# Kernel optimization log

Measured on AMD Instinct MI355X. Metric: run time of the kernel, lower is better.

Reference implementation:

```python
import jax, jax.numpy as jnp
import numpy as np

B, L, J, D_IN, D_OUT = 64, 243, 17, 256, 256
EPS = 1e-5


def _skeleton_adjacency(num_joints=17):
    edges = [(0, 1), (1, 2), (2, 3), (0, 4), (4, 5), (5, 6), (0, 7), (7, 8), (8, 9),
             (9, 10), (8, 11), (11, 12), (12, 13), (1, 14), (14, 15), (1, 16), (16, 17)]
    adj = np.zeros((num_joints, num_joints), dtype=np.float32)
    for u, v in edges:
        if u < num_joints and v < num_joints:
            adj[u, v] = 1.0
            adj[v, u] = 1.0
    np.fill_diagonal(adj, 1.0)
    d = adj.sum(axis=1) ** (-0.5)
    return (d[:, None] * adj) * d[None, :]


def setup_inputs() -> dict:
    key = jax.random.key(0)
    ks = jax.random.split(key, 8)
    s_in = 1.0 / np.sqrt(D_IN)
    s_out = 1.0 / np.sqrt(D_OUT)
    s_h = 1.0 / np.sqrt(2 * D_OUT)
    return {
        "x": jax.random.normal(ks[0], (B, L, J, D_IN), dtype=jnp.float32),
        "adj": jnp.asarray(_skeleton_adjacency(J)),
        "w1": jax.random.normal(ks[1], (D_OUT, D_IN), dtype=jnp.float32) * s_in,
        "b1": jnp.zeros((D_OUT,), dtype=jnp.float32),
        "w2": jax.random.normal(ks[2], (D_OUT, D_IN), dtype=jnp.float32) * s_in,
        "b2": jnp.zeros((D_OUT,), dtype=jnp.float32),
        "bn_gamma": jnp.ones((D_OUT,), dtype=jnp.float32),
        "bn_beta": jnp.zeros((D_OUT,), dtype=jnp.float32),
        "ln_gamma": jnp.ones((D_OUT,), dtype=jnp.float32),
        "ln_beta": jnp.zeros((D_OUT,), dtype=jnp.float32),
        "mlp_w1": jax.random.normal(ks[3], (2 * D_OUT, D_OUT), dtype=jnp.float32) * s_out,
        "mlp_b1": jnp.zeros((2 * D_OUT,), dtype=jnp.float32),
        "mlp_w2": jax.random.normal(ks[4], (D_OUT, 2 * D_OUT), dtype=jnp.float32) * s_h,
        "mlp_b2": jnp.zeros((D_OUT,), dtype=jnp.float32),
    }


def reference(x, adj, w1, b1, w2, b2, bn_gamma, bn_beta, ln_gamma, ln_beta,
              mlp_w1, mlp_b1, mlp_w2, mlp_b2):
    b, l, j, d = x.shape
    xf = x.reshape(b * l, j, d)  # [BL, J, D]
    # two linear projections, each aggregated over joints by the (symmetric)
    # normalized adjacency: out1 uses adj^T, out2 uses adj
    o1 = jnp.einsum("njd,od->njo", xf, w1) + b1
    o1 = jnp.einsum("ji,njo->nio", adj, o1)  # adj.T aggregation
    o2 = jnp.einsum("njd,od->njo", xf, w2) + b2
    o2 = jnp.einsum("ij,njo->nio", adj, o2)
    h = jax.nn.relu(o1 + o2)  # [BL, J, Dout]
    # BatchNorm1d over flattened (BL*J) rows, biased variance (training mode)
    mu = h.mean(axis=(0, 1))
    var = jnp.mean(jnp.square(h - mu), axis=(0, 1))
    h = (h - mu) * jax.lax.rsqrt(var + EPS) * bn_gamma + bn_beta
    # LayerNorm over channel dim
    lmu = h.mean(axis=-1, keepdims=True)
    lvar = jnp.mean(jnp.square(h - lmu), axis=-1, keepdims=True)
    hn = (h - lmu) * jax.lax.rsqrt(lvar + EPS) * ln_gamma + ln_beta
    # MLP: Linear -> ReLU -> Linear
    mid = jax.nn.relu(jnp.einsum("njo,ho->njh", hn, mlp_w1) + mlp_b1)
    out = jnp.einsum("njh,oh->njo", mid, mlp_w2) + mlp_b2
    return out.reshape(b, l, j, -1)
```

## Files before the change

### kernel.cpp

```cpp
#include <hip/hip_runtime.h>
#include <hip/hip_bf16.h>

#define NGRP 15552
#define RROWS 264384
#define EPSV 1e-5f

typedef __attribute__((ext_vector_type(8))) short s16x8;
typedef __attribute__((ext_vector_type(4))) float f32x4;
typedef __hip_bfloat16 bf16;

__device__ __forceinline__ float bf2f(unsigned short u) {
    union { unsigned int i; float f; } x; x.i = ((unsigned int)u) << 16; return x.f;
}
__device__ __forceinline__ unsigned short f2bf(float f) {
    bf16 b = __float2bfloat16(f);
    return *reinterpret_cast<unsigned short*>(&b);
}

__global__ __launch_bounds__(256)
void k_prep(const float* __restrict__ w1, const float* __restrict__ b1,
            const float* __restrict__ w2, const float* __restrict__ b2,
            const float* __restrict__ mw1, const float* __restrict__ mw2,
            const float* __restrict__ adj,
            bf16* __restrict__ wsum, bf16* __restrict__ w1m, bf16* __restrict__ w2m,
            float* __restrict__ bsum, float* __restrict__ srow, float* __restrict__ stats)
{
    const int idx = blockIdx.x * 256 + threadIdx.x;
    if (idx < 65536) wsum[idx] = __float2bfloat16(w1[idx] + w2[idx]);
    w1m[idx] = __float2bfloat16(mw1[idx]);
    w2m[idx] = __float2bfloat16(mw2[idx]);
    if (idx < 256) bsum[idx] = b1[idx] + b2[idx];
    if (idx < 512) stats[idx] = 0.0f;
    if (idx < 17) {
        float s = 0.0f;
        for (int j = 0; j < 17; ++j) s += adj[idx * 17 + j];
        srow[idx] = s;
    }
}

__global__ __launch_bounds__(256)
void k_agg(const float* __restrict__ x, const float* __restrict__ adj,
           bf16* __restrict__ xa)
{
    __shared__ float sadj[289];
    const int t = threadIdx.x;
    sadj[t < 289 ? t : 0] = adj[t < 289 ? t : 0];
    if (t < 33) sadj[256 + t] = adj[256 + t];
    __syncthreads();
    const size_t base = (size_t)blockIdx.x * (17 * 256) + t;
    float xv[17];
#pragma unroll
    for (int j = 0; j < 17; ++j) xv[j] = x[base + j * 256];
#pragma unroll
    for (int i = 0; i < 17; ++i) {
        float s = 0.0f;
#pragma unroll
        for (int j = 0; j < 17; ++j) s = fmaf(sadj[i * 17 + j], xv[j], s);
        xa[base + i * 256] = __float2bfloat16(s);
    }
}

template<int KDIM, int EPI>
__global__ __launch_bounds__(256, 2)
void gemm_bt(const bf16* __restrict__ A, const bf16* __restrict__ Bw,
             void* __restrict__ Cout, int M,
             const float* __restrict__ bias, const float* __restrict__ srow)
{
    constexpr int LDK = 72;
    __shared__ bf16 sA[128 * LDK];
    __shared__ bf16 sB[128 * LDK];
    const int tid  = threadIdx.x;
    const int wave = tid >> 6, lane = tid & 63;
    const int wm = (wave >> 1) * 64, wn = (wave & 1) * 64;
    const int quad = lane >> 4, l16 = lane & 15;
    const int m0 = blockIdx.y * 128;
    const int n0 = blockIdx.x * 128;
    const int ldc = gridDim.x * 128;

    f32x4 acc[4][4] = {};

    const int str = tid >> 3;
    const int stc = (tid & 7) * 8;

    for (int kt = 0; kt < KDIM / 64; ++kt) {
        const int k0 = kt * 64;
#pragma unroll
        for (int i = 0; i < 4; ++i) {
            const int r = str + i * 32;
            int gr = m0 + r; gr = gr < M ? gr : M - 1;
            *(uint4*)(sA + r * LDK + stc) =
                *(const uint4*)(A + (size_t)gr * KDIM + k0 + stc);
        }
#pragma unroll
        for (int i = 0; i < 4; ++i) {
            const int r = str + i * 32;
            *(uint4*)(sB + r * LDK + stc) =
                *(const uint4*)(Bw + (size_t)(n0 + r) * KDIM + k0 + stc);
        }
        __syncthreads();
#pragma unroll
        for (int ks = 0; ks < 2; ++ks) {
            const int kk = ks * 32 + quad * 8;
            s16x8 af[4], bfr[4];
#pragma unroll
            for (int xx = 0; xx < 4; ++xx)
                af[xx] = *(const s16x8*)(sA + (wm + xx * 16 + l16) * LDK + kk);
#pragma unroll
            for (int xx = 0; xx < 4; ++xx)
                bfr[xx] = *(const s16x8*)(sB + (wn + xx * 16 + l16) * LDK + kk);
#pragma unroll
            for (int i = 0; i < 4; ++i)
#pragma unroll
                for (int j = 0; j < 4; ++j)
                    acc[i][j] = __builtin_amdgcn_mfma_f32_16x16x32_bf16(
                        af[i], bfr[j], acc[i][j], 0, 0, 0);
        }
        __syncthreads();
    }

#pragma unroll
    for (int j = 0; j < 4; ++j) {
        const int col = n0 + wn + j * 16 + l16;
        const float bc = bias[col];
#pragma unroll
        for (int i = 0; i < 4; ++i) {
            const int rb = m0 + wm + i * 16 + quad * 4;
#pragma unroll
            for (int r = 0; r < 4; ++r) {
                const int row = rb + r;
                if (row < M) {
                    float v = acc[i][j][r];
                    if constexpr (EPI == 0) {
                        v += srow[row % 17] * bc;
                        v = fmaxf(v, 0.0f);
                        ((bf16*)Cout)[(size_t)row * ldc + col] = __float2bfloat16(v);
                    } else if constexpr (EPI == 1) {
                        v += bc;
                        v = fmaxf(v, 0.0f);
                        ((bf16*)Cout)[(size_t)row * ldc + col] = __float2bfloat16(v);
                    } else {
                        v += bc;
                        ((float*)Cout)[(size_t)row * ldc + col] = v;
                    }
                }
            }
        }
    }
}

__global__ __launch_bounds__(256)
void k_stats(const bf16* __restrict__ h, float* __restrict__ stats)
{
    const int t  = threadIdx.x;
    const int c0 = (t & 127) * 2;
    const int rs = t >> 7;
    float s0 = 0, s1 = 0, q0 = 0, q1 = 0;
    for (int r = blockIdx.x * 2 + rs; r < RROWS; r += 1024) {
        const ushort2 u = *(const ushort2*)(h + (size_t)r * 256 + c0);
        const float v0 = bf2f(u.x), v1 = bf2f(u.y);
        s0 += v0; q0 += v0 * v0;
        s1 += v1; q1 += v1 * v1;
    }
    atomicAdd(&stats[c0], s0);
    atomicAdd(&stats[c0 + 1], s1);
    atomicAdd(&stats[256 + c0], q0);
    atomicAdd(&stats[256 + c0 + 1], q1);
}

__global__ __launch_bounds__(256)
void k_norm(const bf16* __restrict__ h, bf16* __restrict__ hn,
            const float* __restrict__ stats,
            const float* __restrict__ bng, const float* __restrict__ bnb,
            const float* __restrict__ lng, const float* __restrict__ lnb)
{
    __shared__ float sm[256], sv[256], sg[256], sb[256], sl[256], so[256];
    const int t = threadIdx.x;
    {
        const float mu  = stats[t] * (1.0f / RROWS);
        const float var = stats[256 + t] * (1.0f / RROWS) - mu * mu;
        sm[t] = mu; sv[t] = rsqrtf(var + EPSV);
        sg[t] = bng[t]; sb[t] = bnb[t]; sl[t] = lng[t]; so[t] = lnb[t];
    }
    __syncthreads();
    const int wave = t >> 6, lane = t & 63;
    const int c = lane * 4;
    float mn[4], rs[4], gg[4], bb[4], lg[4], lb[4];
#pragma unroll
    for (int k = 0; k < 4; ++k) {
        mn[k] = sm[c + k]; rs[k] = sv[c + k]; gg[k] = sg[c + k];
        bb[k] = sb[c + k]; lg[k] = sl[c + k]; lb[k] = so[c + k];
    }
    for (int row = blockIdx.x * 4 + wave; row < RROWS; row += 8192) {
        const ushort4 u = *(const ushort4*)(h + (size_t)row * 256 + c);
        float v[4] = { bf2f(u.x), bf2f(u.y), bf2f(u.z), bf2f(u.w) };
        float s = 0.0f, q = 0.0f;
#pragma unroll
        for (int k = 0; k < 4; ++k) {
            v[k] = (v[k] - mn[k]) * rs[k] * gg[k] + bb[k];
            s += v[k]; q += v[k] * v[k];
        }
#pragma unroll
        for (int off = 32; off > 0; off >>= 1) {
            s += __shfl_xor(s, off);
            q += __shfl_xor(q, off);
        }
        const float lmu = s * (1.0f / 256.0f);
        const float lrs = rsqrtf(q * (1.0f / 256.0f) - lmu * lmu + EPSV);
        ushort4 o;
        o.x = f2bf((v[0] - lmu) * lrs * lg[0] + lb[0]);
        o.y = f2bf((v[1] - lmu) * lrs * lg[1] + lb[1]);
        o.z = f2bf((v[2] - lmu) * lrs * lg[2] + lb[2]);
        o.w = f2bf((v[3] - lmu) * lrs * lg[3] + lb[3]);
        *(ushort4*)(hn + (size_t)row * 256 + c) = o;
    }
}

extern "C" void kernel_launch(void* const* d_in, const int* in_sizes, int n_in,
                              void* d_out, int out_size, void* d_ws, size_t ws_size,
                              hipStream_t stream)
{
    const float* x   = (const float*)d_in[0];
    const float* adj = (const float*)d_in[1];
    const float* w1  = (const float*)d_in[2];
    const float* b1  = (const float*)d_in[3];
    const float* w2  = (const float*)d_in[4];
    const float* b2  = (const float*)d_in[5];
    const float* bng = (const float*)d_in[6];
    const float* bnb = (const float*)d_in[7];
    const float* lng = (const float*)d_in[8];
    const float* lnb = (const float*)d_in[9];
    const float* mw1 = (const float*)d_in[10];
    const float* mb1 = (const float*)d_in[11];
    const float* mw2 = (const float*)d_in[12];
    const float* mb2 = (const float*)d_in[13];

    char* ws = (char*)d_ws;
    const size_t SZ1 = (size_t)RROWS * 256 * 2;
    bf16* xa  = (bf16*)(ws);
    bf16* h   = (bf16*)(ws + SZ1);
    bf16* mid = (bf16*)(ws + SZ1);
    char* wp  = ws + SZ1 + (size_t)RROWS * 512 * 2;
    bf16*  wsum  = (bf16*)(wp);
    bf16*  w1m   = (bf16*)(wp + 131072);
    bf16*  w2m   = (bf16*)(wp + 131072 + 262144);
    float* bsum  = (float*)(wp + 131072 + 262144 + 262144);
    float* srow  = (float*)((char*)bsum + 1024);
    float* stats = (float*)((char*)srow + 128);

    const int mt = (RROWS + 127) / 128;

    k_prep<<<512, 256, 0, stream>>>(w1, b1, w2, b2, mw1, mw2, adj,
                                    wsum, w1m, w2m, bsum, srow, stats);
    k_agg<<<NGRP, 256, 0, stream>>>(x, adj, xa);
    gemm_bt<256, 0><<<dim3(2, mt), 256, 0, stream>>>(xa, wsum, h, RROWS, bsum, srow);
    k_stats<<<512, 256, 0, stream>>>(h, stats);
    k_norm<<<2048, 256, 0, stream>>>(h, xa, stats, bng, bnb, lng, lnb);
    gemm_bt<256, 1><<<dim3(4, mt), 256, 0, stream>>>(xa, w1m, mid, RROWS, mb1, nullptr);
    gemm_bt<512, 2><<<dim3(2, mt), 256, 0, stream>>>(mid, w2m, d_out, RROWS, mb2, nullptr);
}
```

Before: 1.161 ms.

## Fuse MLP GEMMs into one kernel and stage GEMM epilogue through LDS

Replaces the two separate MLP GEMMs with a single kernel that keeps a 64-row tile of normalized activations and the 512-wide hidden intermediate in shared memory, so the bf16 mid tensor never goes to global memory. Weights are read directly from global/L2 per wave rather than staged through LDS. The first GEMM's epilogue now writes results to shared memory and then stores them as coalesced 16-byte rows instead of scattered 2-byte stores. The fused kernel gives up the LDS reuse of weight tiles and uses a smaller M tile, which may raise L2 traffic and lower MFMA efficiency.

```diff
diff --git a/kernel.cpp b/kernel.cpp
--- a/kernel.cpp
+++ b/kernel.cpp
@@ -60,42 +60,43 @@
     }
 }
 
-template<int KDIM, int EPI>
 __global__ __launch_bounds__(256, 2)
-void gemm_bt(const bf16* __restrict__ A, const bf16* __restrict__ Bw,
-             void* __restrict__ Cout, int M,
-             const float* __restrict__ bias, const float* __restrict__ srow)
+void gemm_h(const bf16* __restrict__ A, const bf16* __restrict__ Bw,
+            bf16* __restrict__ H, const float* __restrict__ bias,
+            const float* __restrict__ srow)
 {
     constexpr int LDK = 72;
-    __shared__ bf16 sA[128 * LDK];
-    __shared__ bf16 sB[128 * LDK];
+    constexpr int LDC = 136;
+    __shared__ char smem[2 * 128 * LDK * 2];
+    bf16* const sA = (bf16*)smem;
+    bf16* const sB = sA + 128 * LDK;
+    bf16* const sC = (bf16*)smem;
+
     const int tid  = threadIdx.x;
     const int wave = tid >> 6, lane = tid & 63;
     const int wm = (wave >> 1) * 64, wn = (wave & 1) * 64;
     const int quad = lane >> 4, l16 = lane & 15;
     const int m0 = blockIdx.y * 128;
     const int n0 = blockIdx.x * 128;
-    const int ldc = gridDim.x * 128;
 
     f32x4 acc[4][4] = {};
-
     const int str = tid >> 3;
     const int stc = (tid & 7) * 8;
 
-    for (int kt = 0; kt < KDIM / 64; ++kt) {
+    for (int kt = 0; kt < 4; ++kt) {
         const int k0 = kt * 64;
 #pragma unroll
         for (int i = 0; i < 4; ++i) {
             const int r = str + i * 32;
-            int gr = m0 + r; gr = gr < M ? gr : M - 1;
+            int gr = m0 + r; gr = gr < RROWS ? gr : RROWS - 1;
             *(uint4*)(sA + r * LDK + stc) =
-                *(const uint4*)(A + (size_t)gr * KDIM + k0 + stc);
+                *(const uint4*)(A + (size_t)gr * 256 + k0 + stc);
         }
 #pragma unroll
         for (int i = 0; i < 4; ++i) {
             const int r = str + i * 32;
             *(uint4*)(sB + r * LDK + stc) =
-                *(const uint4*)(Bw + (size_t)(n0 + r) * KDIM + k0 + stc);
+                *(const uint4*)(Bw + (size_t)(n0 + r) * 256 + k0 + stc);
         }
         __syncthreads();
 #pragma unroll
@@ -103,11 +104,11 @@
             const int kk = ks * 32 + quad * 8;
             s16x8 af[4], bfr[4];
 #pragma unroll
-            for (int xx = 0; xx < 4; ++xx)
-                af[xx] = *(const s16x8*)(sA + (wm + xx * 16 + l16) * LDK + kk);
-#pragma unroll
-            for (int xx = 0; xx < 4; ++xx)
-                bfr[xx] = *(const s16x8*)(sB + (wn + xx * 16 + l16) * LDK + kk);
+            for (int x = 0; x < 4; ++x)
+                af[x] = *(const s16x8*)(sA + (wm + x * 16 + l16) * LDK + kk);
+#pragma unroll
+            for (int x = 0; x < 4; ++x)
+                bfr[x] = *(const s16x8*)(sB + (wn + x * 16 + l16) * LDK + kk);
 #pragma unroll
             for (int i = 0; i < 4; ++i)
 #pragma unroll
@@ -120,30 +121,28 @@
 
 #pragma unroll
     for (int j = 0; j < 4; ++j) {
-        const int col = n0 + wn + j * 16 + l16;
-        const float bc = bias[col];
+        const int cl = wn + j * 16 + l16;
+        const float bc = bias[n0 + cl];
 #pragma unroll
         for (int i = 0; i < 4; ++i) {
-            const int rb = m0 + wm + i * 16 + quad * 4;
 #pragma unroll
             for (int r = 0; r < 4; ++r) {
-                const int row = rb + r;
-                if (row < M) {
-                    float v = acc[i][j][r];
-                    if constexpr (EPI == 0) {
-                        v += srow[row % 17] * bc;
-                        v = fmaxf(v, 0.0f);
-                        ((bf16*)Cout)[(size_t)row * ldc + col] = __float2bfloat16(v);
-                    } else if constexpr (EPI == 1) {
-                        v += bc;
-                        v = fmaxf(v, 0.0f);
-                        ((bf16*)Cout)[(size_t)row * ldc + col] = __float2bfloat16(v);
-                    } else {
-                        v += bc;
-                        ((float*)Cout)[(size_t)row * ldc + col] = v;
-                    }
-                }
+                const int lr = wm + i * 16 + quad * 4 + r;
+                const int gr = m0 + lr;
+                float v = acc[i][j][r] + srow[gr % 17] * bc;
+                v = fmaxf(v, 0.0f);
+                sC[lr * LDC + cl] = __float2bfloat16(v);
             }
+        }
+    }
+    __syncthreads();
+    const int row = tid >> 1;
+    const int cb  = (tid & 1) * 64;
+    if (m0 + row < RROWS) {
+#pragma unroll
+        for (int k = 0; k < 8; ++k) {
+            uint4 u = *(const uint4*)(sC + row * LDC + cb + k * 8);
+            *(uint4*)(H + (size_t)(m0 + row) * 256 + n0 + cb + k * 8) = u;
         }
     }
 }
@@ -212,6 +211,110 @@
         o.z = f2bf((v[2] - lmu) * lrs * lg[2] + lb[2]);
         o.w = f2bf((v[3] - lmu) * lrs * lg[3] + lb[3]);
         *(ushort4*)(hn + (size_t)row * 256 + c) = o;
+    }
+}
+
+__global__ __launch_bounds__(256, 2)
+void k_mlp2(const bf16* __restrict__ hng, const bf16* __restrict__ w1m,
+            const float* __restrict__ mb1, const bf16* __restrict__ w2m,
+            const float* __restrict__ mb2, float* __restrict__ out)
+{
+    constexpr int LDH = 264;
+    constexpr int LDO = 260;
+    __shared__ char smemB[64 * LDH * 2 * 2];
+    bf16* const hn  = (bf16*)smemB;
+    bf16* const mid = hn + 64 * LDH;
+    float* const oc = (float*)smemB;
+
+    const int tid  = threadIdx.x;
+    const int wave = tid >> 6, lane = tid & 63;
+    const int quad = lane >> 4, l16 = lane & 15;
+    const int m0 = blockIdx.x * 64;
+
+    {
+        const int r = tid >> 2, c = (tid & 3) * 64;
+        const bf16* src = hng + (size_t)(m0 + r) * 256 + c;
+#pragma unroll
+        for (int k = 0; k < 8; ++k)
+            *(uint4*)(hn + r * LDH + c + k * 8) = *(const uint4*)(src + k * 8);
+    }
+    __syncthreads();
+
+    const int wn = wave * 64;
+    f32x4 aco[4][4] = {};
+
+    for (int hh = 0; hh < 2; ++hh) {
+        f32x4 acm[4][4] = {};
+#pragma unroll 2
+        for (int ks = 0; ks < 8; ++ks) {
+            const int kk = ks * 32 + quad * 8;
+            s16x8 af[4], bw[4];
+#pragma unroll
+            for (int j = 0; j < 4; ++j)
+                bw[j] = *(const s16x8*)(w1m + (size_t)(hh * 256 + wn + j * 16 + l16) * 256 + kk);
+#pragma unroll
+            for (int i = 0; i < 4; ++i)
+                af[i] = *(const s16x8*)(hn + (i * 16 + l16) * LDH + kk);
+#pragma unroll
+            for (int i = 0; i < 4; ++i)
+#pragma unroll
+                for (int j = 0; j < 4; ++j)
+                    acm[i][j] = __builtin_amdgcn_mfma_f32_16x16x32_bf16(
+                        af[i], bw[j], acm[i][j], 0, 0, 0);
+        }
+        __syncthreads();
+#pragma unroll
+        for (int j = 0; j < 4; ++j) {
+            const int cl = wn + j * 16 + l16;
+            const float bc = mb1[hh * 256 + cl];
+#pragma unroll
+            for (int i = 0; i < 4; ++i)
+#pragma unroll
+                for (int r = 0; r < 4; ++r) {
+                    float v = acm[i][j][r] + bc;
+                    mid[(i * 16 + quad * 4 + r) * LDH + cl] =
+                        __float2bfloat16(fmaxf(v, 0.0f));
+                }
+        }
+        __syncthreads();
+#pragma unroll 2
+        for (int ks = 0; ks < 8; ++ks) {
+            const int kk = ks * 32 + quad * 8;
+            s16x8 af[4], bw[4];
+#pragma unroll
+            for (int j = 0; j < 4; ++j)
+                bw[j] = *(const s16x8*)(w2m + (size_t)(wn + j * 16 + l16) * 512 + hh * 256 + kk);
+#pragma unroll
+            for (int i = 0; i < 4; ++i)
+                af[i] = *(const s16x8*)(mid + (i * 16 + l16) * LDH + kk);
+#pragma unroll
+            for (int i = 0; i < 4; ++i)
+#pragma unroll
+                for (int j = 0; j < 4; ++j)
+                    aco[i][j] = __builtin_amdgcn_mfma_f32_16x16x32_bf16(
+                        af[i], bw[j], aco[i][j], 0, 0, 0);
+        }
+        __syncthreads();
+    }
+
+#pragma unroll
+    for (int j = 0; j < 4; ++j) {
+        const int cl = wn + j * 16 + l16;
+        const float bc = mb2[cl];
+#pragma unroll
+        for (int i = 0; i < 4; ++i)
+#pragma unroll
+            for (int r = 0; r < 4; ++r)
+                oc[(i * 16 + quad * 4 + r) * LDO + cl] = aco[i][j][r] + bc;
+    }
+    __syncthreads();
+    const int row = tid >> 2;
+    const int cb2 = (tid & 3) * 64;
+    const size_t gb = (size_t)(m0 + row) * 256 + cb2;
+#pragma unroll
+    for (int k = 0; k < 16; ++k) {
+        f32x4 u = *(const f32x4*)(oc + row * LDO + cb2 + k * 4);
+        *(f32x4*)(out + gb + k * 4) = u;
     }
 }
 
@@ -236,10 +339,9 @@
 
     char* ws = (char*)d_ws;
     const size_t SZ1 = (size_t)RROWS * 256 * 2;
-    bf16* xa  = (bf16*)(ws);
-    bf16* h   = (bf16*)(ws + SZ1);
-    bf16* mid = (bf16*)(ws + SZ1);
-    char* wp  = ws + SZ1 + (size_t)RROWS * 512 * 2;
+    bf16* xa = (bf16*)(ws);
+    bf16* h  = (bf16*)(ws + SZ1);
+    char* wp = ws + 2 * SZ1;
     bf16*  wsum  = (bf16*)(wp);
     bf16*  w1m   = (bf16*)(wp + 131072);
     bf16*  w2m   = (bf16*)(wp + 131072 + 262144);
@@ -247,14 +349,11 @@
     float* srow  = (float*)((char*)bsum + 1024);
     float* stats = (float*)((char*)srow + 128);
 
-    const int mt = (RROWS + 127) / 128;
-
     k_prep<<<512, 256, 0, stream>>>(w1, b1, w2, b2, mw1, mw2, adj,
                                     wsum, w1m, w2m, bsum, srow, stats);
     k_agg<<<NGRP, 256, 0, stream>>>(x, adj, xa);
-    gemm_bt<256, 0><<<dim3(2, mt), 256, 0, stream>>>(xa, wsum, h, RROWS, bsum, srow);
+    gemm_h<<<dim3(2, 2066), 256, 0, stream>>>(xa, wsum, h, bsum, srow);
     k_stats<<<512, 256, 0, stream>>>(h, stats);
     k_norm<<<2048, 256, 0, stream>>>(h, xa, stats, bng, bnb, lng, lnb);
-    gemm_bt<256, 1><<<dim3(4, mt), 256, 0, stream>>>(xa, w1m, mid, RROWS, mb1, nullptr);
-    gemm_bt<512, 2><<<dim3(2, mt), 256, 0, stream>>>(mid, w2m, d_out, RROWS, mb2, nullptr);
-}
+    k_mlp2<<<RROWS / 64, 256, 0, stream>>>(xa, w1m, mb1, w2m, mb2, (float*)d_out);
+}
```

Measured after the change: 1.125 ms. 3.1% less time.
